# Performance work log

Measured on AMD Instinct MI355X. Metric: run time of the kernel, lower is better.

## Reference

```python
import jax, jax.numpy as jnp
import numpy as np

CHF_STEP = 30       # frequency half-span in steps
CHF_TIK = 0.01      # frequency spacing per step
SAMPLE_STEP = 1.0   # image-plane sampling interval
SCALE = 1.0


def _make_templates(H, W, dtype):
    # sample coordinates of the flattened (transposed) map: n = w*H + h
    half = SAMPLE_STEP / 2
    x_axis = jnp.linspace(half, W * SAMPLE_STEP - half, W, dtype=dtype)
    y_axis = jnp.linspace(half, H * SAMPLE_STEP - half, H, dtype=dtype)
    coords = jnp.stack([jnp.repeat(x_axis, H), jnp.tile(y_axis, W)], axis=0)  # [2, N]
    freqs = jnp.arange(-CHF_STEP, CHF_STEP, dtype=dtype) * CHF_TIK            # [2S]
    S2 = 2 * CHF_STEP
    # plane[i, j] = (freqs[j], freqs[i])  -> angle[i,j,n] = freqs[j]*x[n] + freqs[i]*y[n]
    angle = (freqs[None, :, None] * coords[0][None, None, :]
             + freqs[:, None, None] * coords[1][None, None, :])  # [2S, 2S, N]
    return jnp.cos(angle), jnp.sin(angle)


def _chf(flat_map, real_t, img_t):
    # dense contraction over the N pixel axis (a skinny GEMM)
    chf_real = jnp.einsum('ijn,bn->bij', real_t, flat_map)
    chf_img = jnp.einsum('ijn,bn->bij', img_t, flat_map)
    return jnp.stack([chf_real, chf_img], axis=-1)  # [B, 2S, 2S, 2]


def setup_inputs() -> dict:
    key = jax.random.key(0)
    k1, k2 = jax.random.split(key)
    B, H, W = 8, 64, 64
    dnn_output = jax.random.uniform(k1, (B, H, W), dtype=jnp.float32)
    gt_density_map = jax.random.uniform(k2, (B, H, W), dtype=jnp.float32)
    return {"dnn_output": dnn_output, "gt_density_map": gt_density_map}


def reference(dnn_output, gt_density_map):
    B, H, W = dnn_output.shape
    real_t, img_t = _make_templates(H, W, dnn_output.dtype)
    # flatten in (W-major, H-minor) order to match transpose(-1,-2).view(B,-1)
    flat_out = jnp.swapaxes(dnn_output, -1, -2).reshape(B, -1)   # [B, N]
    flat_gt = jnp.swapaxes(gt_density_map, -1, -2).reshape(B, -1)
    derived_chf = _chf(flat_out, real_t, img_t)   # [B, 2S, 2S, 2]
    gt_chf = _chf(flat_gt, real_t, img_t)         # [B, 2S, 2S, 2]
    # squared-error likelihood between derived and GT characteristic functions
    loss = jnp.mean(jnp.sum((derived_chf - gt_chf) ** 2, axis=(1, 2, 3))) * SCALE
    return loss
```

## Files before the change

### kernel.cpp

```cpp
#include <hip/hip_runtime.h>
#include <hip/hip_bf16.h>


#define S2   60
#define HW   64
#define NPIX 4096
#define NB   8

__global__ void chf_tables_kernel(float2* __restrict__ ey, float2* __restrict__ exT) {
    int idx = blockIdx.x * blockDim.x + threadIdx.x;
    if (idx < S2 * HW) {
        int i = idx >> 6, h = idx & 63;
        float f = (float)(i - 30) * 0.01f;
        float s, c;
        sincosf(f * ((float)h + 0.5f), &s, &c);
        ey[idx] = make_float2(c, s);
    } else if (idx < 2 * S2 * HW) {
        int k = idx - S2 * HW;
        int w = k / S2, j = k - w * S2;
        float f = (float)(j - 30) * 0.01f;
        float s, c;
        sincosf(f * ((float)w + 0.5f), &s, &c);
        exT[k] = make_float2(c, s);
    }
}

template <bool USE_WS>
__global__ __launch_bounds__(64) void chf_loss_kernel(
        const float* __restrict__ dnn, const float* __restrict__ gt,
        const float2* __restrict__ ey_g, const float2* __restrict__ exT_g,
        float* __restrict__ out) {
    __shared__ float eyr[HW], eyi[HW];
    __shared__ float Tr[HW], Ti[HW];
    __shared__ float exr[USE_WS ? 1 : S2 * HW];
    __shared__ float exi[USE_WS ? 1 : S2 * HW];

    const int t = threadIdx.x;
    const int b = blockIdx.x / S2;
    const int i = blockIdx.x - b * S2;

    if (USE_WS) {
        float2 e = ey_g[i * HW + t];
        eyr[t] = e.x; eyi[t] = e.y;
    } else {
        float f = (float)(i - 30) * 0.01f;
        float s, c;
        sincosf(f * ((float)t + 0.5f), &s, &c);
        eyr[t] = c; eyi[t] = s;
        for (int k = t; k < S2 * HW; k += 64) {
            int w = k / S2, j = k - w * S2;
            float fj = (float)(j - 30) * 0.01f;
            float sj, cj;
            sincosf(fj * ((float)w + 0.5f), &sj, &cj);
            exr[k] = cj; exi[k] = sj;
        }
    }
    __syncthreads();

    const float* __restrict__ pd = dnn + b * NPIX;
    const float* __restrict__ pg = gt + b * NPIX;
    float tr = 0.f, ti = 0.f;
#pragma unroll 8
    for (int h = 0; h < HW; ++h) {
        float d = pd[h * HW + t] - pg[h * HW + t];
        tr = fmaf(eyr[h], d, tr);
        ti = fmaf(eyi[h], d, ti);
    }
    Tr[t] = tr; Ti[t] = ti;
    __syncthreads();

    float acc = 0.f;
    if (t < S2) {
        float cr = 0.f, ci = 0.f;
#pragma unroll 8
        for (int w = 0; w < HW; ++w) {
            float c, s;
            if (USE_WS) {
                float2 e = exT_g[w * S2 + t];
                c = e.x; s = e.y;
            } else {
                c = exr[w * S2 + t];
                s = exi[w * S2 + t];
            }
            float ar = Tr[w], ai = Ti[w];
            cr = fmaf(c, ar, cr);
            cr = fmaf(-s, ai, cr);
            ci = fmaf(c, ai, ci);
            ci = fmaf(s, ar, ci);
        }
        acc = fmaf(cr, cr, ci * ci);
    }

#pragma unroll
    for (int off = 32; off > 0; off >>= 1)
        acc += __shfl_down(acc, off);

    if (t == 0)
        atomicAdd(out, acc * (1.0f / (float)NB));
}

extern "C" void kernel_launch(void* const* d_in, const int* in_sizes, int n_in,
                              void* d_out, int out_size, void* d_ws, size_t ws_size,
                              hipStream_t stream) {
    const float* dnn = (const float*)d_in[0];
    const float* gt  = (const float*)d_in[1];
    float* out = (float*)d_out;

    hipMemsetAsync(out, 0, (size_t)out_size * sizeof(float), stream);

    const size_t table_bytes = (size_t)(2 * S2 * HW) * sizeof(float2);
    if (ws_size >= table_bytes) {
        float2* ey  = (float2*)d_ws;
        float2* exT = ey + S2 * HW;
        int n = 2 * S2 * HW;
        chf_tables_kernel<<<(n + 255) / 256, 256, 0, stream>>>(ey, exT);
        chf_loss_kernel<true><<<NB * S2, 64, 0, stream>>>(dnn, gt, ey, exT, out);
    } else {
        chf_loss_kernel<false><<<NB * S2, 64, 0, stream>>>(dnn, gt, nullptr, nullptr, out);
    }
}
```

Before: 68.12 us.

## Replace precomputed x-phase table with rotation recurrence and drop table kernel

Removes the separate table-generation kernel and its workspace reads. The x-direction phase factors are now generated on the fly with a complex rotation recurrence (two sincosf calls, then one multiply per step), so the whole loss runs as a single kernel. This cuts one launch and the global reads of the table. In exchange, the recurrence adds a little rounding drift over 64 steps and puts a serial dependency into the inner loop.

```diff
diff --git a/kernel.cpp b/kernel.cpp
--- a/kernel.cpp
+++ b/kernel.cpp
@@ -7,53 +7,21 @@
 #define NPIX 4096
 #define NB   8
 
-__global__ void chf_tables_kernel(float2* __restrict__ ey, float2* __restrict__ exT) {
-    int idx = blockIdx.x * blockDim.x + threadIdx.x;
-    if (idx < S2 * HW) {
-        int i = idx >> 6, h = idx & 63;
-        float f = (float)(i - 30) * 0.01f;
-        float s, c;
-        sincosf(f * ((float)h + 0.5f), &s, &c);
-        ey[idx] = make_float2(c, s);
-    } else if (idx < 2 * S2 * HW) {
-        int k = idx - S2 * HW;
-        int w = k / S2, j = k - w * S2;
-        float f = (float)(j - 30) * 0.01f;
-        float s, c;
-        sincosf(f * ((float)w + 0.5f), &s, &c);
-        exT[k] = make_float2(c, s);
-    }
-}
-
-template <bool USE_WS>
-__global__ __launch_bounds__(64) void chf_loss_kernel(
+__global__ __launch_bounds__(64) void chf_loss_fused(
         const float* __restrict__ dnn, const float* __restrict__ gt,
-        const float2* __restrict__ ey_g, const float2* __restrict__ exT_g,
         float* __restrict__ out) {
     __shared__ float eyr[HW], eyi[HW];
     __shared__ float Tr[HW], Ti[HW];
-    __shared__ float exr[USE_WS ? 1 : S2 * HW];
-    __shared__ float exi[USE_WS ? 1 : S2 * HW];
 
     const int t = threadIdx.x;
     const int b = blockIdx.x / S2;
     const int i = blockIdx.x - b * S2;
 
-    if (USE_WS) {
-        float2 e = ey_g[i * HW + t];
-        eyr[t] = e.x; eyi[t] = e.y;
-    } else {
-        float f = (float)(i - 30) * 0.01f;
+    {
+        float fi = (float)(i - 30) * 0.01f;
         float s, c;
-        sincosf(f * ((float)t + 0.5f), &s, &c);
+        sincosf(fi * ((float)t + 0.5f), &s, &c);
         eyr[t] = c; eyi[t] = s;
-        for (int k = t; k < S2 * HW; k += 64) {
-            int w = k / S2, j = k - w * S2;
-            float fj = (float)(j - 30) * 0.01f;
-            float sj, cj;
-            sincosf(fj * ((float)w + 0.5f), &sj, &cj);
-            exr[k] = cj; exi[k] = sj;
-        }
     }
     __syncthreads();
 
@@ -71,22 +39,21 @@
 
     float acc = 0.f;
     if (t < S2) {
+        float fj = (float)(t - 30) * 0.01f;
+        float sc, cc, sd, cd;
+        sincosf(fj * 0.5f, &sc, &cc);
+        sincosf(fj, &sd, &cd);
         float cr = 0.f, ci = 0.f;
 #pragma unroll 8
         for (int w = 0; w < HW; ++w) {
-            float c, s;
-            if (USE_WS) {
-                float2 e = exT_g[w * S2 + t];
-                c = e.x; s = e.y;
-            } else {
-                c = exr[w * S2 + t];
-                s = exi[w * S2 + t];
-            }
             float ar = Tr[w], ai = Ti[w];
-            cr = fmaf(c, ar, cr);
-            cr = fmaf(-s, ai, cr);
-            ci = fmaf(c, ai, ci);
-            ci = fmaf(s, ar, ci);
+            cr = fmaf(cc, ar, cr);
+            cr = fmaf(-sc, ai, cr);
+            ci = fmaf(cc, ai, ci);
+            ci = fmaf(sc, ar, ci);
+            float cn = fmaf(cc, cd, -(sc * sd));
+            float sn = fmaf(sc, cd, cc * sd);
+            cc = cn; sc = sn;
         }
         acc = fmaf(cr, cr, ci * ci);
     }
@@ -108,14 +75,5 @@
 
     hipMemsetAsync(out, 0, (size_t)out_size * sizeof(float), stream);
 
-    const size_t table_bytes = (size_t)(2 * S2 * HW) * sizeof(float2);
-    if (ws_size >= table_bytes) {
-        float2* ey  = (float2*)d_ws;
-        float2* exT = ey + S2 * HW;
-        int n = 2 * S2 * HW;
-        chf_tables_kernel<<<(n + 255) / 256, 256, 0, stream>>>(ey, exT);
-        chf_loss_kernel<true><<<NB * S2, 64, 0, stream>>>(dnn, gt, ey, exT, out);
-    } else {
-        chf_loss_kernel<false><<<NB * S2, 64, 0, stream>>>(dnn, gt, nullptr, nullptr, out);
-    }
+    chf_loss_fused<<<NB * S2, 64, 0, stream>>>(dnn, gt, out);
 }
```

Result: faster. 66.23 us (-2.8%).
